# Kernel tuning notes

Measured on AMD Instinct MI355X. Metric: run time of the kernel, lower is better.

## Reference

```python
import jax, jax.numpy as jnp
import numpy as np

L = 16          # hash-grid levels (opt.L)
F = 2           # features per level
N_MIN = 16      # base resolution
T = 1 << 19     # hashmap size per level (log2_T = 19, bound == 1)
BOUND = 1.0
B = float(np.exp(np.log(512.0 / 16.0) / (L - 1)))  # per-level scale
PRIMES = np.array([1, 2654435761, 805459861], dtype=np.uint32)
# 8 corner offsets of the trilinear cell, in {0,1}^3
OFFS = np.array([[i, j, k] for i in (0, 1) for j in (0, 1) for k in (0, 1)], dtype=np.float32)


def hash_grid_encode(xn, tables):
    """xn: [N,3] in [0,1]; tables: [L,T,F]. Returns [N, L*F]."""
    offs_f = jnp.asarray(OFFS)                      # [8,3] float
    offs_u = jnp.asarray(OFFS.astype(np.uint32))    # [8,3] uint32
    primes = jnp.asarray(PRIMES)
    feats = []
    for l in range(L):
        res = int(np.floor(N_MIN * B ** l))
        pos = xn * res                              # [N,3]
        pf = jnp.minimum(jnp.floor(pos), float(res - 1))
        frac = pos - pf                             # [N,3], grads flow to x
        base = pf.astype(jnp.uint32)                # [N,3]
        corners = base[:, None, :] + offs_u[None]   # [N,8,3]
        if (res + 1) ** 3 <= T:
            # grid fits in table: coherent dense indexing (tcnn behavior)
            stride = jnp.asarray(np.array([1, res + 1, (res + 1) ** 2], dtype=np.uint32))
            idx = (corners * stride).sum(-1)        # [N,8]
        else:
            h = corners * primes                    # uint32 wraps (mod 2^32)
            idx = (h[..., 0] ^ h[..., 1] ^ h[..., 2]) & jnp.uint32(T - 1)
        vals = tables[l, idx.astype(jnp.int32)]     # [N,8,F] gather
        w = jnp.prod(jnp.where(offs_f[None] > 0, frac[:, None, :], 1.0 - frac[:, None, :]), axis=-1)  # [N,8]
        feats.append(jnp.einsum('nc,ncf->nf', w, vals))
    return jnp.concatenate(feats, axis=-1)          # [N, L*F]


def _wn(v, g):
    # torch weight_norm, dim=0: per-output-row normalization
    return g[:, None] * v / jnp.linalg.norm(v, axis=1, keepdims=True)


def setup_inputs() -> dict:
    key = jax.random.key(0)
    k = jax.random.split(key, 4)
    N = 2097152
    x = jax.random.uniform(k[0], (N, 3), jnp.float32, -BOUND, BOUND)
    tables = jax.random.normal(k[1], (L, T, F), jnp.float32) * 1e-2
    v1 = jax.random.normal(k[2], (64, L * F), jnp.float32) * (1.0 / np.sqrt(L * F))
    g1 = jnp.ones((64,), jnp.float32)
    b1 = jnp.zeros((64,), jnp.float32)
    v2 = jax.random.normal(k[3], (3, 64), jnp.float32) * (1.0 / 8.0)
    g2 = jnp.ones((3,), jnp.float32)
    b2 = jnp.zeros((3,), jnp.float32)
    return {"x": x, "tables": tables, "v1": v1, "g1": g1, "b1": b1,
            "v2": v2, "g2": g2, "b2": b2}


def reference(x, tables, v1, g1, b1, v2, g2, b2):
    xn = (x + BOUND) / (2.0 * BOUND)                # map to [0,1]
    h = hash_grid_encode(xn, tables)                # [N, 32]
    h1 = jax.nn.relu(h @ _wn(v1, g1).T + b1)        # [N, 64]
    out = jnp.tanh(h1 @ _wn(v2, g2).T + b2)         # [N, 3]
    return out
```

## Files before the change

### kernel.cpp

```cpp
#include <hip/hip_runtime.h>
#include <math.h>

#define LVL 16
#define TBL (1u << 19)
#define PR1 2654435761u
#define PR2 805459861u
#define NDENSE 7
#define NHASH 9

typedef __attribute__((ext_vector_type(4))) float f4;
typedef __attribute__((ext_vector_type(4))) unsigned u4;
typedef __attribute__((ext_vector_type(8))) short bf16x8;
typedef __attribute__((ext_vector_type(4))) float f32x4;

union FragU { unsigned u[4]; bf16x8 v; };

struct EncParams {
    float resf[LVL];
    float resm1[LVL];
    unsigned s1[LVL];
    unsigned s2[LVL];
    unsigned dense_mask;
};

struct FinalParams {
    float resf[NDENSE];
    float resm1[NDENSE];
    unsigned cellbase[NDENSE];
    unsigned cres[NDENSE];
    unsigned cres2[NDENSE];
};

struct CellBuild {
    unsigned nc[NDENSE];
    unsigned res[NDENSE];
    unsigned s1[NDENSE], s2[NDENSE];
    unsigned dst_dw[NDENSE];
};

static __device__ __forceinline__ unsigned f2bf(float f) {
    unsigned u = __float_as_uint(f);
    u += 0x7FFFu + ((u >> 16) & 1u);
    return u >> 16;
}
static __device__ __forceinline__ float bf_lo(unsigned p) { return __uint_as_float(p << 16); }
static __device__ __forceinline__ float bf_hi(unsigned p) { return __uint_as_float(p & 0xFFFF0000u); }

static __device__ __forceinline__ float fast_tanh(float v) {
    v = fminf(fmaxf(v, -10.f), 10.f);
    float e = __expf(2.0f * v);
    return __fdividef(e - 1.0f, e + 1.0f);
}

static __device__ __forceinline__ void gather8_sc0(const unsigned* __restrict__ tb,
                                                   const unsigned* off, unsigned* val)
{
    asm volatile(
        "global_load_dword %0, %8, %16 sc0\n\t"
        "global_load_dword %1, %9, %16 sc0\n\t"
        "global_load_dword %2, %10, %16 sc0\n\t"
        "global_load_dword %3, %11, %16 sc0\n\t"
        "global_load_dword %4, %12, %16 sc0\n\t"
        "global_load_dword %5, %13, %16 sc0\n\t"
        "global_load_dword %6, %14, %16 sc0\n\t"
        "global_load_dword %7, %15, %16 sc0\n\t"
        "s_waitcnt vmcnt(0)"
        : "=&v"(val[0]), "=&v"(val[1]), "=&v"(val[2]), "=&v"(val[3]),
          "=&v"(val[4]), "=&v"(val[5]), "=&v"(val[6]), "=&v"(val[7])
        : "v"(off[0]), "v"(off[1]), "v"(off[2]), "v"(off[3]),
          "v"(off[4]), "v"(off[5]), "v"(off[6]), "v"(off[7]),
          "s"(tb)
        : "memory");
}

static __device__ __forceinline__ void gather4x2_sc0(const unsigned* __restrict__ tb,
                                                     const unsigned* off,
                                                     unsigned long long* val)
{
    asm volatile(
        "global_load_dwordx2 %0, %4, %8 sc0\n\t"
        "global_load_dwordx2 %1, %5, %8 sc0\n\t"
        "global_load_dwordx2 %2, %6, %8 sc0\n\t"
        "global_load_dwordx2 %3, %7, %8 sc0\n\t"
        "s_waitcnt vmcnt(0)"
        : "=&v"(val[0]), "=&v"(val[1]), "=&v"(val[2]), "=&v"(val[3])
        : "v"(off[0]), "v"(off[1]), "v"(off[2]), "v"(off[3]),
          "s"(tb)
        : "memory");
}

static __device__ __forceinline__ void gather10x4_sc0(const unsigned* __restrict__ tb,
                                                      const unsigned* off, u4* val)
{
    asm volatile(
        "global_load_dwordx4 %0, %10, %20 sc0\n\t"
        "global_load_dwordx4 %1, %11, %20 sc0\n\t"
        "global_load_dwordx4 %2, %12, %20 sc0\n\t"
        "global_load_dwordx4 %3, %13, %20 sc0\n\t"
        "global_load_dwordx4 %4, %14, %20 sc0\n\t"
        "global_load_dwordx4 %5, %15, %20 sc0\n\t"
        "global_load_dwordx4 %6, %16, %20 sc0\n\t"
        "global_load_dwordx4 %7, %17, %20 sc0\n\t"
        "global_load_dwordx4 %8, %18, %20 sc0\n\t"
        "global_load_dwordx4 %9, %19, %20 sc0\n\t"
        "s_waitcnt vmcnt(0)"
        : "=&v"(val[0]), "=&v"(val[1]), "=&v"(val[2]), "=&v"(val[3]), "=&v"(val[4]),
          "=&v"(val[5]), "=&v"(val[6]), "=&v"(val[7]), "=&v"(val[8]), "=&v"(val[9])
        : "v"(off[0]), "v"(off[1]), "v"(off[2]), "v"(off[3]), "v"(off[4]),
          "v"(off[5]), "v"(off[6]), "v"(off[7]), "v"(off[8]), "v"(off[9]),
          "s"(tb)
        : "memory");
}

static __device__ __forceinline__ void gather4x4_sc0(const unsigned* __restrict__ tb,
                                                     const unsigned* off, u4* val)
{
    asm volatile(
        "global_load_dwordx4 %0, %4, %8 sc0\n\t"
        "global_load_dwordx4 %1, %5, %8 sc0\n\t"
        "global_load_dwordx4 %2, %6, %8 sc0\n\t"
        "global_load_dwordx4 %3, %7, %8 sc0\n\t"
        "s_waitcnt vmcnt(0)"
        : "=&v"(val[0]), "=&v"(val[1]), "=&v"(val[2]), "=&v"(val[3])
        : "v"(off[0]), "v"(off[1]), "v"(off[2]), "v"(off[3]),
          "s"(tb)
        : "memory");
}

__global__ __launch_bounds__(256)
void prep_weights(const float* __restrict__ v1, const float* __restrict__ g1,
                  const float* __restrict__ v2, const float* __restrict__ g2,
                  float* __restrict__ ws)
{
    int t = threadIdx.x;
    if (t < 64) {
        float row[32];
        float s = 0.f;
        for (int i = 0; i < 32; ++i) { row[i] = v1[t * 32 + i]; s += row[i] * row[i]; }
        float sc = g1[t] / sqrtf(s);
        unsigned* wbf = (unsigned*)ws + 2304;
        for (int i = 0; i < 32; ++i) ws[t * 32 + i] = row[i] * sc;
        for (int w = 0; w < 16; ++w)
            wbf[t * 16 + w] = (f2bf(row[2 * w + 1] * sc) << 16) | f2bf(row[2 * w] * sc);
    } else if (t < 67) {
        int r = t - 64;
        float s = 0.f;
        for (int i = 0; i < 64; ++i) { float v = v2[r * 64 + i]; s += v * v; }
        float scale = g2[r] / sqrtf(s);
        for (int i = 0; i < 64; ++i) ws[2048 + r * 64 + i] = v2[r * 64 + i] * scale;
    }
}

__global__ __launch_bounds__(256)
void convert_tables(const float* __restrict__ src, unsigned* __restrict__ dst, int npairs)
{
    int j = blockIdx.x * 256 + threadIdx.x;
    if (j >= npairs) return;
    f4 v = __builtin_nontemporal_load((const f4*)src + j);
    unsigned lo = (f2bf(v.y) << 16) | f2bf(v.x);
    unsigned hi = (f2bf(v.w) << 16) | f2bf(v.z);
    unsigned long long o = ((unsigned long long)hi << 32) | lo;
    __builtin_nontemporal_store(o, (unsigned long long*)dst + j);
}

__global__ __launch_bounds__(256)
void build_cell(const float* __restrict__ tables, unsigned* __restrict__ region, CellBuild cb)
{
    int l = blockIdx.y;
    unsigned c = blockIdx.x * 256 + threadIdx.x;
    if (c >= cb.nc[l]) return;
    unsigned res = cb.res[l];
    unsigned cx = c % res, t = c / res;
    unsigned cy = t % res, cz = t / res;
    unsigned s1 = cb.s1[l], s2 = cb.s2[l];
    unsigned base = cx + cy * s1 + cz * s2;
    const float* src = tables + (size_t)l * TBL * 2;
    unsigned o[8];
#pragma unroll
    for (int k = 0; k < 8; ++k) {
        unsigned e = base + (k & 1u) + ((k >> 1) & 1u) * s1 + (k >> 2) * s2;
        o[k] = (f2bf(src[2 * e + 1]) << 16) | f2bf(src[2 * e]);
    }
    u4* dst = (u4*)(region + cb.dst_dw[l] + 8u * c);
    u4 o0 = {o[0], o[1], o[2], o[3]};
    u4 o1 = {o[4], o[5], o[6], o[7]};
    dst[0] = o0; dst[1] = o1;
}

__global__ __launch_bounds__(256, 4)
void encode_hash4(const float* __restrict__ x, const unsigned* __restrict__ tb,
                  unsigned* __restrict__ hout, int N, float rf, float rm1)
{
    int j = blockIdx.x * 256 + threadIdx.x;
    int i0 = 4 * j;
    if (i0 >= N) return;

    if (i0 + 4 <= N) {
        const f4* xp = (const f4*)(x + (size_t)3 * i0);
        f4 q0 = __builtin_nontemporal_load(xp);
        f4 q1 = __builtin_nontemporal_load(xp + 1);
        f4 q2 = __builtin_nontemporal_load(xp + 2);
        float n0[4], n1[4], n2[4];
        n0[0] = (q0.x + 1.f) * 0.5f; n1[0] = (q0.y + 1.f) * 0.5f; n2[0] = (q0.z + 1.f) * 0.5f;
        n0[1] = (q0.w + 1.f) * 0.5f; n1[1] = (q1.x + 1.f) * 0.5f; n2[1] = (q1.y + 1.f) * 0.5f;
        n0[2] = (q1.z + 1.f) * 0.5f; n1[2] = (q1.w + 1.f) * 0.5f; n2[2] = (q2.x + 1.f) * 0.5f;
        n0[3] = (q2.y + 1.f) * 0.5f; n1[3] = (q2.z + 1.f) * 0.5f; n2[3] = (q2.w + 1.f) * 0.5f;

        unsigned o[4];
#pragma unroll
        for (int p = 0; p < 4; ++p) {
            float a0 = n0[p] * rf, a1 = n1[p] * rf, a2 = n2[p] * rf;
            float w0 = fminf(floorf(a0), rm1);
            float w1 = fminf(floorf(a1), rm1);
            float w2 = fminf(floorf(a2), rm1);
            float f0 = a0 - w0, f1 = a1 - w1, f2 = a2 - w2;
            unsigned c0 = (unsigned)w0;
            unsigned hx0 = c0, hx1 = c0 + 1u;
            unsigned hy0 = (unsigned)w1 * PR1, hy1 = hy0 + PR1;
            unsigned hz0 = (unsigned)w2 * PR2, hz1 = hz0 + PR2;

            float acc0, acc1;
            if (!(c0 & 1u)) {
                unsigned pb[4], qq[4];
#pragma unroll
                for (int jj = 0; jj < 4; ++jj) {
                    unsigned hyv = (jj & 2) ? hy1 : hy0;
                    unsigned hzv = (jj & 1) ? hz1 : hz0;
                    unsigned idx0 = (hx0 ^ hyv ^ hzv) & (TBL - 1u);
                    qq[jj] = idx0 & 1u;
                    pb[jj] = (idx0 & ~1u) << 2;
                }
                unsigned long long pv[4];
                gather4x2_sc0(tb, pb, pv);
                float wx1 = f0, wx0 = 1.f - f0;
                acc0 = 0.f; acc1 = 0.f;
#pragma unroll
                for (int jj = 0; jj < 4; ++jj) {
                    unsigned lo = (unsigned)pv[jj];
                    unsigned hi = (unsigned)(pv[jj] >> 32);
                    unsigned x0 = qq[jj] ? hi : lo;
                    unsigned x1 = qq[jj] ? lo : hi;
                    float wyz = ((jj & 2) ? f1 : 1.f - f1) * ((jj & 1) ? f2 : 1.f - f2);
                    acc0 = fmaf(wyz, fmaf(wx0, bf_lo(x0), wx1 * bf_lo(x1)), acc0);
                    acc1 = fmaf(wyz, fmaf(wx0, bf_hi(x0), wx1 * bf_hi(x1)), acc1);
                }
            } else {
                unsigned off[8];
#pragma unroll
                for (int c = 0; c < 8; ++c) {
                    unsigned hx = (c & 4) ? hx1 : hx0;
                    unsigned hy = (c & 2) ? hy1 : hy0;
                    unsigned hz = (c & 1) ? hz1 : hz0;
                    off[c] = ((hx ^ hy ^ hz) & (TBL - 1u)) << 2;
                }
                unsigned v[8];
                gather8_sc0(tb, off, v);
                acc0 = 0.f; acc1 = 0.f;
#pragma unroll
                for (int c = 0; c < 8; ++c) {
                    float w = ((c & 4) ? f0 : 1.f - f0) *
                              ((c & 2) ? f1 : 1.f - f1) *
                              ((c & 1) ? f2 : 1.f - f2);
                    acc0 = fmaf(w, bf_lo(v[c]), acc0);
                    acc1 = fmaf(w, bf_hi(v[c]), acc1);
                }
            }
            o[p] = (f2bf(acc1) << 16) | f2bf(acc0);
        }
        u4 ov = {o[0], o[1], o[2], o[3]};
        __builtin_nontemporal_store(ov, (u4*)(hout + i0));
    } else {
        for (int i = i0; i < N; ++i) {
            float xn0 = (x[3 * i + 0] + 1.0f) * 0.5f;
            float xn1 = (x[3 * i + 1] + 1.0f) * 0.5f;
            float xn2 = (x[3 * i + 2] + 1.0f) * 0.5f;
            float p0 = xn0 * rf, p1 = xn1 * rf, p2 = xn2 * rf;
            float pf0 = fminf(floorf(p0), rm1), pf1 = fminf(floorf(p1), rm1), pf2 = fminf(floorf(p2), rm1);
            float fg0 = p0 - pf0, fg1 = p1 - pf1, fg2 = p2 - pf2;
            unsigned hx0 = (unsigned)pf0, hx1 = hx0 + 1u;
            unsigned hy0 = (unsigned)pf1 * PR1, hy1 = hy0 + PR1;
            unsigned hz0 = (unsigned)pf2 * PR2, hz1 = hz0 + PR2;
            float a0 = 0.f, a1 = 0.f;
#pragma unroll
            for (int c = 0; c < 8; ++c) {
                unsigned hxv = (c & 4) ? hx1 : hx0;
                unsigned hyv = (c & 2) ? hy1 : hy0;
                unsigned hzv = (c & 1) ? hz1 : hz0;
                unsigned vv = tb[(hxv ^ hyv ^ hzv) & (TBL - 1u)];
                float w = ((c & 4) ? fg0 : 1.f - fg0) * ((c & 2) ? fg1 : 1.f - fg1) * ((c & 1) ? fg2 : 1.f - fg2);
                a0 = fmaf(w, bf_lo(vv), a0);
                a1 = fmaf(w, bf_hi(vv), a1);
            }
            hout[i] = (f2bf(a1) << 16) | f2bf(a0);
        }
    }
}

static __device__ __forceinline__ unsigned blend_cell(u4 e0, u4 e1,
                                                      float fx, float fy, float fz)
{
    float wx1 = fx, wx0 = 1.f - fx;
    float wy1 = fy, wy0 = 1.f - fy;
    float lo0 = wy0 * fmaf(wx0, bf_lo(e0[0]), wx1 * bf_lo(e0[1]))
              + wy1 * fmaf(wx0, bf_lo(e0[2]), wx1 * bf_lo(e0[3]));
    float hi0 = wy0 * fmaf(wx0, bf_hi(e0[0]), wx1 * bf_hi(e0[1]))
              + wy1 * fmaf(wx0, bf_hi(e0[2]), wx1 * bf_hi(e0[3]));
    float lo1 = wy0 * fmaf(wx0, bf_lo(e1[0]), wx1 * bf_lo(e1[1]))
              + wy1 * fmaf(wx0, bf_lo(e1[2]), wx1 * bf_lo(e1[3]));
    float hi1 = wy0 * fmaf(wx0, bf_hi(e1[0]), wx1 * bf_hi(e1[1]))
              + wy1 * fmaf(wx0, bf_hi(e1[2]), wx1 * bf_hi(e1[3]));
    float acc0 = fmaf(fz, lo1 - lo0, lo0);
    float acc1 = fmaf(fz, hi1 - hi0, hi0);
    acc0 = (1.f - fz) * lo0 + fz * lo1;
    acc1 = (1.f - fz) * hi0 + fz * hi1;
    return (f2bf(acc1) << 16) | f2bf(acc0);
}

__global__ __launch_bounds__(256, 4)
void final_mfma(const float* __restrict__ x, const unsigned* __restrict__ tb,
                const unsigned* __restrict__ hbuf, const unsigned* __restrict__ w1bf,
                const float* __restrict__ b1, const float* __restrict__ w2,
                const float* __restrict__ b2, float* __restrict__ out,
                int N, FinalParams dp)
{
    __shared__ unsigned lds[256 * 20];
    int tid = threadIdx.x;
    int i = blockIdx.x * 256 + tid;

    unsigned hp[NHASH];
#pragma unroll
    for (int l = 0; l < NHASH; ++l)
        hp[l] = __builtin_nontemporal_load(hbuf + (size_t)l * N + i);

    float xn0 = (__builtin_nontemporal_load(x + 3 * i + 0) + 1.0f) * 0.5f;
    float xn1 = (__builtin_nontemporal_load(x + 3 * i + 1) + 1.0f) * 0.5f;
    float xn2 = (__builtin_nontemporal_load(x + 3 * i + 2) + 1.0f) * 0.5f;

    float fr[NDENSE][3];
    unsigned offs[2 * NDENSE];
#pragma unroll
    for (int l = 0; l < NDENSE; ++l) {
        float rf = dp.resf[l];
        float p0 = xn0 * rf, p1 = xn1 * rf, p2 = xn2 * rf;
        float pf0 = fminf(floorf(p0), dp.resm1[l]);
        float pf1 = fminf(floorf(p1), dp.resm1[l]);
        float pf2 = fminf(floorf(p2), dp.resm1[l]);
        fr[l][0] = p0 - pf0; fr[l][1] = p1 - pf1; fr[l][2] = p2 - pf2;
        unsigned c = (unsigned)pf0 + (unsigned)pf1 * dp.cres[l] + (unsigned)pf2 * dp.cres2[l];
        unsigned base = dp.cellbase[l] + c * 32u;
        offs[2 * l + 0] = base;
        offs[2 * l + 1] = base + 16u;
    }

    unsigned hw[16];
    {
        u4 xv[10];
        gather10x4_sc0(tb, offs, xv);
#pragma unroll
        for (int l = 0; l < 5; ++l)
            hw[l] = blend_cell(xv[2 * l], xv[2 * l + 1], fr[l][0], fr[l][1], fr[l][2]);
    }
    {
        u4 yv[4];
        gather4x4_sc0(tb, offs + 10, yv);
        hw[5] = blend_cell(yv[0], yv[1], fr[5][0], fr[5][1], fr[5][2]);
        hw[6] = blend_cell(yv[2], yv[3], fr[6][0], fr[6][1], fr[6][2]);
    }
#pragma unroll
    for (int l = 0; l < NHASH; ++l) hw[NDENSE + l] = hp[l];

    unsigned* row = &lds[tid * 20];
#pragma unroll
    for (int c = 0; c < 4; ++c)
        *(uint4*)(row + 4 * c) = make_uint4(hw[4 * c], hw[4 * c + 1], hw[4 * c + 2], hw[4 * c + 3]);

    __syncthreads();

    int lane = tid & 63;
    int wv   = tid >> 6;
    int l16  = lane & 15;
    int lhi  = lane >> 4;

    bf16x8 bfr[4];
#pragma unroll
    for (int t = 0; t < 4; ++t) {
        const unsigned* p = w1bf + (t * 16 + l16) * 16 + lhi * 4;
        FragU u;
        u.u[0] = p[0]; u.u[1] = p[1]; u.u[2] = p[2]; u.u[3] = p[3];
        bfr[t] = u.v;
    }
    float b1v[4];
#pragma unroll
    for (int t = 0; t < 4; ++t) b1v[t] = b1[t * 16 + l16];
    float w2v[3][4];
#pragma unroll
    for (int jj = 0; jj < 3; ++jj)
#pragma unroll
        for (int t = 0; t < 4; ++t) w2v[jj][t] = w2[jj * 64 + t * 16 + l16];
    float bias2 = (l16 < 3) ? b2[l16] : 0.f;

#pragma unroll
    for (int g = 0; g < 4; ++g) {
        const unsigned* rp = &lds[(wv * 64 + g * 16 + l16) * 20 + lhi * 4];
        FragU u;
        u.u[0] = rp[0]; u.u[1] = rp[1]; u.u[2] = rp[2]; u.u[3] = rp[3];
        bf16x8 af = u.v;

        f32x4 acc[4];
#pragma unroll
        for (int t = 0; t < 4; ++t) {
            f32x4 z = {0.f, 0.f, 0.f, 0.f};
            acc[t] = __builtin_amdgcn_mfma_f32_16x16x32_bf16(af, bfr[t], z, 0, 0, 0);
        }

#pragma unroll
        for (int r = 0; r < 4; ++r) {
            float p0 = 0.f, p1 = 0.f, p2 = 0.f;
#pragma unroll
            for (int t = 0; t < 4; ++t) {
                float a = fmaxf(acc[t][r] + b1v[t], 0.f);
                p0 = fmaf(a, w2v[0][t], p0);
                p1 = fmaf(a, w2v[1][t], p1);
                p2 = fmaf(a, w2v[2][t], p2);
            }
#pragma unroll
            for (int m = 1; m < 16; m <<= 1) {
                p0 += __shfl_xor(p0, m);
                p1 += __shfl_xor(p1, m);
                p2 += __shfl_xor(p2, m);
            }
            if (l16 < 3) {
                int point = blockIdx.x * 256 + wv * 64 + g * 16 + lhi * 4 + r;
                float v = (l16 == 0) ? p0 : ((l16 == 1) ? p1 : p2);
                out[(size_t)point * 3 + l16] = fast_tanh(v + bias2);
            }
        }
    }
}

__global__ __launch_bounds__(256)
void fused_ngp(const float* __restrict__ x, const float* __restrict__ tables,
               const float* __restrict__ w1, const float* __restrict__ b1,
               const float* __restrict__ w2, const float* __restrict__ b2,
               float* __restrict__ out, int N, EncParams ep)
{
    int i = blockIdx.x * 256 + threadIdx.x;
    if (i >= N) return;

    float xn0 = (x[3 * i + 0] + 1.0f) * 0.5f;
    float xn1 = (x[3 * i + 1] + 1.0f) * 0.5f;
    float xn2 = (x[3 * i + 2] + 1.0f) * 0.5f;

    float h[2 * LVL];

#pragma unroll
    for (int l = 0; l < LVL; ++l) {
        float rf = ep.resf[l];
        float p0 = xn0 * rf, p1 = xn1 * rf, p2 = xn2 * rf;
        float pf0 = fminf(floorf(p0), ep.resm1[l]);
        float pf1 = fminf(floorf(p1), ep.resm1[l]);
        float pf2 = fminf(floorf(p2), ep.resm1[l]);
        float fr0 = p0 - pf0, fr1 = p1 - pf1, fr2 = p2 - pf2;
        unsigned c0 = (unsigned)pf0, c1 = (unsigned)pf1, c2 = (unsigned)pf2;
        const float2* tb = (const float2*)tables + (size_t)l * TBL;

        float acc0 = 0.f, acc1 = 0.f;
        if ((ep.dense_mask >> l) & 1u) {
            unsigned s1 = ep.s1[l], s2 = ep.s2[l];
            unsigned b = c0 + c1 * s1 + c2 * s2;
#pragma unroll
            for (int c = 0; c < 8; ++c) {
                unsigned id = b + ((c & 4) ? 1u : 0u) + ((c & 2) ? s1 : 0u) + ((c & 1) ? s2 : 0u);
                float2 v = tb[id];
                float w = ((c & 4) ? fr0 : 1.f - fr0) * ((c & 2) ? fr1 : 1.f - fr1) * ((c & 1) ? fr2 : 1.f - fr2);
                acc0 = fmaf(w, v.x, acc0);
                acc1 = fmaf(w, v.y, acc1);
            }
        } else {
            unsigned hx0 = c0, hx1 = c0 + 1u;
            unsigned hy0 = c1 * PR1, hy1 = hy0 + PR1;
            unsigned hz0 = c2 * PR2, hz1 = hz0 + PR2;
#pragma unroll
            for (int c = 0; c < 8; ++c) {
                unsigned hx = (c & 4) ? hx1 : hx0;
                unsigned hy = (c & 2) ? hy1 : hy0;
                unsigned hz = (c & 1) ? hz1 : hz0;
                float2 v = tb[(hx ^ hy ^ hz) & (TBL - 1u)];
                float w = ((c & 4) ? fr0 : 1.f - fr0) * ((c & 2) ? fr1 : 1.f - fr1) * ((c & 1) ? fr2 : 1.f - fr2);
                acc0 = fmaf(w, v.x, acc0);
                acc1 = fmaf(w, v.y, acc1);
            }
        }
        h[2 * l + 0] = acc0;
        h[2 * l + 1] = acc1;
    }

    float r0 = b2[0], r1 = b2[1], r2 = b2[2];
    for (int o = 0; o < 64; ++o) {
        float a = b1[o];
#pragma unroll
        for (int k = 0; k < 32; ++k) a = fmaf(h[k], w1[o * 32 + k], a);
        a = fmaxf(a, 0.f);
        r0 = fmaf(a, w2[0 * 64 + o], r0);
        r1 = fmaf(a, w2[1 * 64 + o], r1);
        r2 = fmaf(a, w2[2 * 64 + o], r2);
    }
    out[3 * i + 0] = tanhf(r0);
    out[3 * i + 1] = tanhf(r1);
    out[3 * i + 2] = tanhf(r2);
}

extern "C" void kernel_launch(void* const* d_in, const int* in_sizes, int n_in,
                              void* d_out, int out_size, void* d_ws, size_t ws_size,
                              hipStream_t stream)
{
    const float* x      = (const float*)d_in[0];
    const float* tables = (const float*)d_in[1];
    const float* v1     = (const float*)d_in[2];
    const float* g1     = (const float*)d_in[3];
    const float* b1     = (const float*)d_in[4];
    const float* v2     = (const float*)d_in[5];
    const float* g2     = (const float*)d_in[6];
    const float* b2     = (const float*)d_in[7];
    float* out = (float*)d_out;
    float* ws  = (float*)d_ws;
    int N = in_sizes[0] / 3;

    EncParams ep;
    double Bd = exp(log(512.0 / 16.0) / (double)(LVL - 1));
    unsigned dm = 0;
    int resv[LVL];
    for (int l = 0; l < LVL; ++l) {
        int res = (int)floor(16.0 * pow(Bd, (double)l));
        resv[l] = res;
        ep.resf[l]  = (float)res;
        ep.resm1[l] = (float)(res - 1);
        long long rp1 = (long long)res + 1;
        if (rp1 * rp1 * rp1 <= (long long)TBL) dm |= (1u << l);
        ep.s1[l] = (unsigned)(res + 1);
        ep.s2[l] = (unsigned)((res + 1) * (res + 1));
    }
    ep.dense_mask = dm;

    prep_weights<<<1, 256, 0, stream>>>(v1, g1, v2, g2, ws);

    size_t tb_off_bytes = 16384;
    unsigned NC[NDENSE];
    for (int l = 0; l < NDENSE; ++l) {
        unsigned r = (unsigned)resv[l];
        NC[l] = r * r * r;
    }
    bool cell_ok = true;
    for (int l = 0; l < 5; ++l) if (8ull * NC[l] > TBL) cell_ok = false;

    unsigned cum_dw = LVL * TBL;
    cum_dw = (cum_dw + 15u) & ~15u;
    unsigned cell5_dw = cum_dw; cum_dw += (8u * NC[5] + 15u) & ~15u;
    unsigned cell6_dw = cum_dw; cum_dw += (8u * NC[6] + 15u) & ~15u;
    size_t h_off_bytes = tb_off_bytes + (size_t)cum_dw * 4;
    size_t need = h_off_bytes + (size_t)NHASH * (size_t)N * 4;

    bool fast = (ws_size >= need) && (dm == 0x7Fu) && (N % 1024 == 0) && cell_ok;
    if (fast) {
        unsigned* tb   = (unsigned*)((char*)d_ws + tb_off_bytes);
        unsigned* hbuf = (unsigned*)((char*)d_ws + h_off_bytes);
        unsigned* w1bf = (unsigned*)ws + 2304;

        int npairs = (int)((size_t)LVL * TBL / 2);
        convert_tables<<<(npairs + 255) / 256, 256, 0, stream>>>(tables, tb, npairs);

        CellBuild cb;
        unsigned maxNC = 0;
        for (int l = 0; l < NDENSE; ++l) {
            cb.nc[l] = NC[l]; cb.res[l] = (unsigned)resv[l];
            cb.s1[l] = ep.s1[l]; cb.s2[l] = ep.s2[l];
            cb.dst_dw[l] = (l < 5) ? (unsigned)l * TBL
                                   : ((l == 5) ? cell5_dw : cell6_dw);
            if (NC[l] > maxNC) maxNC = NC[l];
        }
        dim3 cgrid((maxNC + 255) / 256, NDENSE);
        build_cell<<<cgrid, 256, 0, stream>>>(tables, tb, cb);

        int grid4 = N / 1024;
        for (int l = 0; l < NHASH; ++l) {
            int gl = NDENSE + l;
            encode_hash4<<<grid4, 256, 0, stream>>>(
                x, tb + (size_t)gl * TBL, hbuf + (size_t)l * N, N,
                ep.resf[gl], ep.resm1[gl]);
        }

        FinalParams dp;
        for (int l = 0; l < NDENSE; ++l) {
            dp.resf[l] = ep.resf[l]; dp.resm1[l] = ep.resm1[l];
            dp.cellbase[l] = ((l < 5) ? (unsigned)l * TBL
                                      : ((l == 5) ? cell5_dw : cell6_dw)) * 4u;
            dp.cres[l] = (unsigned)resv[l];
            dp.cres2[l] = (unsigned)(resv[l] * resv[l]);
        }
        final_mfma<<<N / 256, 256, 0, stream>>>(x, tb, hbuf, w1bf, b1,
                                                ws + 2048, b2, out, N, dp);
    } else {
        fused_ngp<<<(N + 255) / 256, 256, 0, stream>>>(x, tables, ws, b1, ws + 2048, b2, out, N, ep);
    }
}
```

Before: 567.3 us.

## Widen hash gathers to 16-byte aligned loads, skip dense-level conversion, raise occupancy

```diff
diff --git a/kernel.cpp b/kernel.cpp
--- a/kernel.cpp
+++ b/kernel.cpp
@@ -50,6 +50,12 @@
     v = fminf(fmaxf(v, -10.f), 10.f);
     float e = __expf(2.0f * v);
     return __fdividef(e - 1.0f, e + 1.0f);
+}
+
+static __device__ __forceinline__ unsigned sel4(u4 v, unsigned q) {
+    unsigned t0 = (q & 1u) ? v[1] : v[0];
+    unsigned t1 = (q & 1u) ? v[3] : v[2];
+    return (q & 2u) ? t1 : t0;
 }
 
 static __device__ __forceinline__ void gather8_sc0(const unsigned* __restrict__ tb,
@@ -69,22 +75,6 @@
           "=&v"(val[4]), "=&v"(val[5]), "=&v"(val[6]), "=&v"(val[7])
         : "v"(off[0]), "v"(off[1]), "v"(off[2]), "v"(off[3]),
           "v"(off[4]), "v"(off[5]), "v"(off[6]), "v"(off[7]),
-          "s"(tb)
-        : "memory");
-}
-
-static __device__ __forceinline__ void gather4x2_sc0(const unsigned* __restrict__ tb,
-                                                     const unsigned* off,
-                                                     unsigned long long* val)
-{
-    asm volatile(
-        "global_load_dwordx2 %0, %4, %8 sc0\n\t"
-        "global_load_dwordx2 %1, %5, %8 sc0\n\t"
-        "global_load_dwordx2 %2, %6, %8 sc0\n\t"
-        "global_load_dwordx2 %3, %7, %8 sc0\n\t"
-        "s_waitcnt vmcnt(0)"
-        : "=&v"(val[0]), "=&v"(val[1]), "=&v"(val[2]), "=&v"(val[3])
-        : "v"(off[0]), "v"(off[1]), "v"(off[2]), "v"(off[3]),
           "s"(tb)
         : "memory");
 }
@@ -215,36 +205,37 @@
             float w2 = fminf(floorf(a2), rm1);
             float f0 = a0 - w0, f1 = a1 - w1, f2 = a2 - w2;
             unsigned c0 = (unsigned)w0;
-            unsigned hx0 = c0, hx1 = c0 + 1u;
+            unsigned hx0 = c0;
             unsigned hy0 = (unsigned)w1 * PR1, hy1 = hy0 + PR1;
             unsigned hz0 = (unsigned)w2 * PR2, hz1 = hz0 + PR2;
+            float wx1 = f0, wx0 = 1.f - f0;
 
             float acc0, acc1;
-            if (!(c0 & 1u)) {
-                unsigned pb[4], qq[4];
+            if ((c0 & 3u) != 3u) {
+                unsigned d = (c0 & 1u) ? 3u : 1u;
+                unsigned offb[4], qs[4];
 #pragma unroll
                 for (int jj = 0; jj < 4; ++jj) {
                     unsigned hyv = (jj & 2) ? hy1 : hy0;
                     unsigned hzv = (jj & 1) ? hz1 : hz0;
                     unsigned idx0 = (hx0 ^ hyv ^ hzv) & (TBL - 1u);
-                    qq[jj] = idx0 & 1u;
-                    pb[jj] = (idx0 & ~1u) << 2;
+                    qs[jj] = idx0 & 3u;
+                    offb[jj] = (idx0 & ~3u) << 2;
                 }
-                unsigned long long pv[4];
-                gather4x2_sc0(tb, pb, pv);
-                float wx1 = f0, wx0 = 1.f - f0;
+                u4 bv[4];
+                gather4x4_sc0(tb, offb, bv);
                 acc0 = 0.f; acc1 = 0.f;
 #pragma unroll
                 for (int jj = 0; jj < 4; ++jj) {
-                    unsigned lo = (unsigned)pv[jj];
-                    unsigned hi = (unsigned)(pv[jj] >> 32);
-                    unsigned x0 = qq[jj] ? hi : lo;
-                    unsigned x1 = qq[jj] ? lo : hi;
+                    unsigned q = qs[jj];
+                    unsigned x0v = sel4(bv[jj], q);
+                    unsigned x1v = sel4(bv[jj], q ^ d);
                     float wyz = ((jj & 2) ? f1 : 1.f - f1) * ((jj & 1) ? f2 : 1.f - f2);
-                    acc0 = fmaf(wyz, fmaf(wx0, bf_lo(x0), wx1 * bf_lo(x1)), acc0);
-                    acc1 = fmaf(wyz, fmaf(wx0, bf_hi(x0), wx1 * bf_hi(x1)), acc1);
+                    acc0 = fmaf(wyz, fmaf(wx0, bf_lo(x0v), wx1 * bf_lo(x1v)), acc0);
+                    acc1 = fmaf(wyz, fmaf(wx0, bf_hi(x0v), wx1 * bf_hi(x1v)), acc1);
                 }
             } else {
+                unsigned hx1 = c0 + 1u;
                 unsigned off[8];
 #pragma unroll
                 for (int c = 0; c < 8; ++c) {
@@ -309,14 +300,12 @@
               + wy1 * fmaf(wx0, bf_lo(e1[2]), wx1 * bf_lo(e1[3]));
     float hi1 = wy0 * fmaf(wx0, bf_hi(e1[0]), wx1 * bf_hi(e1[1]))
               + wy1 * fmaf(wx0, bf_hi(e1[2]), wx1 * bf_hi(e1[3]));
-    float acc0 = fmaf(fz, lo1 - lo0, lo0);
-    float acc1 = fmaf(fz, hi1 - hi0, hi0);
-    acc0 = (1.f - fz) * lo0 + fz * lo1;
-    acc1 = (1.f - fz) * hi0 + fz * hi1;
+    float acc0 = (1.f - fz) * lo0 + fz * lo1;
+    float acc1 = (1.f - fz) * hi0 + fz * hi1;
     return (f2bf(acc1) << 16) | f2bf(acc0);
 }
 
-__global__ __launch_bounds__(256, 4)
+__global__ __launch_bounds__(256, 6)
 void final_mfma(const float* __restrict__ x, const unsigned* __restrict__ tb,
                 const unsigned* __restrict__ hbuf, const unsigned* __restrict__ w1bf,
                 const float* __restrict__ b1, const float* __restrict__ w2,
@@ -566,8 +555,9 @@
         unsigned* hbuf = (unsigned*)((char*)d_ws + h_off_bytes);
         unsigned* w1bf = (unsigned*)ws + 2304;
 
-        int npairs = (int)((size_t)LVL * TBL / 2);
-        convert_tables<<<(npairs + 255) / 256, 256, 0, stream>>>(tables, tb, npairs);
+        int npairs = (int)((size_t)(LVL - NDENSE) * TBL / 2);
+        convert_tables<<<(npairs + 255) / 256, 256, 0, stream>>>(
+            tables + (size_t)NDENSE * TBL * 2, tb + (size_t)NDENSE * TBL, npairs);
 
         CellBuild cb;
         unsigned maxNC = 0;
```

Measured after the change: 590.9 us. 4.2% more time.
